# Kernel tuning notes

Hardware: AMD Instinct MI355X
Metric: run time of the kernel (lower is better)

Reference implementation:

```python
import jax, jax.numpy as jnp
import numpy as np

WIN = 30


def setup_inputs() -> dict:
    key = jax.random.key(0)
    ks = jax.random.split(key, 10)
    B, T, N = 16, 3000, 128
    d, hid, K = 64, 128, 32  # d_model, 2*d_model, n_clusters
    s = lambda k, shape, fan: jax.random.normal(k, shape, jnp.float32) / np.float32(np.sqrt(fan))
    return {
        "x_enc": jax.random.normal(ks[0], (B, T, N), jnp.float32),
        "conv1_w": s(ks[1], (32, 1, 5), 5),
        "conv1_b": jnp.zeros((32,), jnp.float32),
        "conv2_w": s(ks[2], (32, 32, 5), 160),
        "conv2_b": jnp.zeros((32,), jnp.float32),
        "proj_w": s(ks[3], (32, d), 32),
        "proj_b": jnp.zeros((d,), jnp.float32),
        "prototypes": s(ks[4], (K, d), d),
        "Wx": s(ks[5], (d, 4 * hid), d),   # stacked gate input weights, order [i,f,o,g]
        "bx": jnp.zeros((4 * hid,), jnp.float32),
        "Wh": s(ks[6], (hid, 4 * hid), hid),  # stacked gate hidden weights
        "bh": jnp.zeros((4 * hid,), jnp.float32),
        "q_t": jax.random.normal(ks[7], (hid,), jnp.float32),
        "q_s": jax.random.normal(ks[8], (d,), jnp.float32),
        "cls_w": s(ks[9], (hid + d, 1), hid + d),
        "cls_b": jnp.zeros((1,), jnp.float32),
    }


def _forward(x_enc, conv1_w, conv1_b, conv2_w, conv2_b, proj_w, proj_b,
             prototypes, Wx, bx, Wh, bh, q_t, q_s, cls_w, cls_b):
    B, T, N = x_enc.shape
    Wn = T // WIN
    xw = x_enc[:, :Wn * WIN].reshape(B, Wn, WIN, N)  # [B,Wn,L,N]

    # --- dynamic FC graphs: per-window correlation ---
    xm = xw - xw.mean(axis=2, keepdims=True)
    cov = jnp.einsum('bwln,bwlm->bwnm', xm, xm) / (WIN - 1 + 1e-8)
    var = jnp.clip(jnp.diagonal(cov, axis1=-2, axis2=-1), 1e-8, None)
    std = jnp.sqrt(var)
    corr = cov / (std[..., :, None] * std[..., None, :])
    corr = jnp.nan_to_num(0.5 * (corr + jnp.swapaxes(corr, -1, -2)), nan=0.0, posinf=0.0, neginf=0.0)
    eyeN = jnp.eye(N, dtype=corr.dtype)
    A_seq = corr * (1.0 - eyeN) + eyeN  # [B,Wn,N,N]

    # --- SignalRep over all windows at once (eval mode: no dropout) ---
    seq = jnp.transpose(xw, (0, 1, 3, 2)).reshape(B * Wn * N, 1, WIN)
    dn = ('NCH', 'OIH', 'NCH')
    h = jax.nn.relu(jax.lax.conv_general_dilated(seq, conv1_w, (1,), [(2, 2)], dimension_numbers=dn) + conv1_b[None, :, None])
    h = jax.nn.relu(jax.lax.conv_general_dilated(h, conv2_w, (1,), [(2, 2)], dimension_numbers=dn) + conv2_b[None, :, None])
    h = h.mean(-1) @ proj_w + proj_b
    Hs = h.reshape(B, Wn, N, -1)  # [B,Wn,N,d]

    # --- attention graph pooling (batched over windows) ---
    S = jax.nn.softmax(jnp.einsum('bwnf,kf->bwnk', Hs, prototypes), axis=-1)
    Xc = jnp.einsum('bwnk,bwnf->bwkf', S, Hs)            # [B,Wn,K,d]
    AS = jnp.einsum('bwnm,bwml->bwnl', A_seq, S)
    Ac = jnp.einsum('bwnk,bwnl->bwkl', S, AS)            # [B,Wn,K,K]
    Ac = 0.5 * (Ac + jnp.swapaxes(Ac, -1, -2))

    # --- normalize pooled adjacency once (shared by all 8 gate GCNs) ---
    K = Ac.shape[-1]
    Ahat = Ac + jnp.eye(K, dtype=Ac.dtype)
    dinv = jnp.clip(Ahat.sum(-1), 1e-8, None) ** -0.5
    An = dinv[..., :, None] * Ahat * dinv[..., None, :]  # D^-1/2 (A+I) D^-1/2

    # --- TGRL: GCLSTM recurrence with p_list=(1,2) skip-averaging ---
    hid = Wh.shape[0]
    Xs = jnp.swapaxes(Xc, 0, 1)  # [Wn,B,K,d]
    As = jnp.swapaxes(An, 0, 1)  # [Wn,B,K,K]
    H0 = jnp.zeros((B, K, hid), Xc.dtype)
    b_all = bx + bh

    def step(carry, inp):
        H, H2, C, t = carry  # H = H_hist[-1], H2 = H_hist[-2]
        X, A = inp
        # H_prev = (H + sum of applicable H_hist[-p]) / (1 + count)
        coef = jnp.where(t == 0, 1.0, 2.0)
        denom = jnp.where(t == 0, 1.0, jnp.where(t == 1, 2.0, 3.0))
        Hp = (coef * H + H2) / denom
        g = jnp.einsum('bkm,bmh->bkh', A, X @ Wx + Hp @ Wh + b_all)  # fused 4 gates
        gi, gf, go, gc = jnp.split(g, 4, axis=-1)
        Cn = jax.nn.sigmoid(gf) * C + jax.nn.sigmoid(gi) * jnp.tanh(gc)
        Hn = jax.nn.sigmoid(go) * jnp.tanh(Cn)
        return (Hn, H, Cn, t + 1), Hn

    _, H_seq = jax.lax.scan(step, (H0, H0, H0, jnp.int32(0)), (Xs, As))
    H_seq = jnp.swapaxes(H_seq, 0, 1)  # [B,Wn,K,hid]

    # --- temporal attention pooling ---
    def attn_pool(Z, q):
        qn = q / (jnp.linalg.norm(q) + 1e-8)
        w = jax.nn.softmax(Z @ qn, axis=1)  # softmax over time
        return jnp.einsum('bw,bwf->bf', w, Z)

    z_graph = attn_pool(H_seq.mean(2), q_t)   # mean over clusters
    z_signal = attn_pool(Hs.mean(2), q_s)     # mean over nodes
    z = jnp.concatenate([z_graph, z_signal], axis=-1)
    return jax.nn.sigmoid(z @ cls_w + cls_b)  # out_dim == 1 (binary)


def reference(x_enc, conv1_w, conv1_b, conv2_w, conv2_b, proj_w, proj_b,
              prototypes, Wx, bx, Wh, bh, q_t, q_s, cls_w, cls_b):
    return _forward(x_enc, conv1_w, conv1_b, conv2_w, conv2_b, proj_w, proj_b,
                    prototypes, Wx, bx, Wh, bh, q_t, q_s, cls_w, cls_b)
```

## Files before the change

kernel.cpp:

```cpp
#include <hip/hip_runtime.h>

#define B_   16
#define T_   3000
#define N_   128
#define WIN_ 30
#define WN_  100
#define D_   64
#define HID_ 128
#define K_   32
#define G4_  512

typedef unsigned short us;
typedef __attribute__((ext_vector_type(8))) short short8;
typedef __attribute__((ext_vector_type(4))) short short4v;
typedef __attribute__((ext_vector_type(4))) float floatx4;

__device__ __forceinline__ us f2bf(float f) {
    unsigned u = __float_as_uint(f);
    u += 0x7fffu + ((u >> 16) & 1u);
    return (us)(u >> 16);
}
__device__ __forceinline__ float bf2f(us h) {
    return __uint_as_float(((unsigned)h) << 16);
}
__device__ __forceinline__ float rcpa(float x) { return __builtin_amdgcn_rcpf(x); }
__device__ __forceinline__ float ex2(float x) { return __builtin_amdgcn_exp2f(x); }
__device__ __forceinline__ void ldsbar() {
    __asm__ volatile("s_waitcnt lgkmcnt(0)\n\ts_barrier" ::: "memory");
}

#define SC_IFO (-1.4426950408889634f)
#define SC_C   (-2.8853900817779268f)

__global__ __launch_bounds__(256) void conv_kernel(
    const float* __restrict__ x, const float* __restrict__ w1,
    const float* __restrict__ b1, const float* __restrict__ w2,
    const float* __restrict__ b2, const float* __restrict__ pw,
    const float* __restrict__ pb, us* __restrict__ Hs)
{
    __shared__ __align__(16) float xs_all[30 * 128];
    __shared__ __align__(16) us h1s[8 * 36 * 40];
    __shared__ __align__(16) float Ms[128 * 40];
    __shared__ __align__(16) us PwT_hi[64 * 40];
    __shared__ __align__(16) us PwT_lo[64 * 40];
    const int tid = threadIdx.x;
    const int win = blockIdx.x;
    const int b = win / WN_, w = win - b * WN_;
    const float* xb = x + ((size_t)b * T_ + (size_t)w * WIN_) * N_;
    const int lane = tid & 63, wv = tid >> 6;
    const int l15 = lane & 15, quad = lane >> 4;

    {
        const float4* xb4 = (const float4*)xb;
        float4* xs4 = (float4*)xs_all;
        for (int i = tid; i < 960; i += 256) xs4[i] = xb4[i];
    }
    for (int i = tid; i < 2048; i += 256) {
        int co = i >> 6, d = i & 63;
        float v = pw[i];
        us hi = f2bf(v);
        PwT_hi[d * 40 + co] = hi;
        PwT_lo[d * 40 + co] = f2bf(v - bf2f(hi));
    }
    for (int i = tid; i < 1920; i += 256) {
        int s = i / 240, r = i % 240;
        int ti = r / 40, c = r % 40;
        int tp = (ti < 2) ? ti : (30 + ti);
        h1s[(s * 36 + tp) * 40 + c] = 0;
    }
    short8 whf[2][5];
    #pragma unroll
    for (int cot = 0; cot < 2; cot++)
        #pragma unroll
        for (int dk = 0; dk < 5; dk++)
            #pragma unroll
            for (int j = 0; j < 8; j++)
                whf[cot][dk][j] = (short)f2bf(w2[(cot * 16 + l15) * 160 + (quad * 8 + j) * 5 + dk]);
    const float b2c0 = b2[l15], b2c1 = b2[16 + l15];
    const int ci2 = lane & 15, th = (lane >> 4) & 1, sloc = lane >> 5;
    float w1ra[5], w1rb[5];
    #pragma unroll
    for (int k = 0; k < 5; k++) {
        w1ra[k] = w1[(2 * ci2) * 5 + k];
        w1rb[k] = w1[(2 * ci2 + 1) * 5 + k];
    }
    const float b1a = b1[2 * ci2], b1b = b1[2 * ci2 + 1];
    float pbv[4];
    #pragma unroll
    for (int nt = 0; nt < 4; nt++) pbv[nt] = pb[nt * 16 + l15];
    ldsbar();

    for (int g = 0; g < 16; g++) {
        const int n1 = g * 8 + wv * 2 + sloc;
        {
            float xr[19];
            #pragma unroll
            for (int u = 0; u < 19; u++) {
                int p = th * 15 - 2 + u;
                xr[u] = ((unsigned)p < 30u) ? xs_all[p * 128 + n1] : 0.f;
            }
            const int rbase = (wv * 2 + sloc) * 36 + 2 + th * 15;
            #pragma unroll
            for (int tt = 0; tt < 15; tt++) {
                float aa = b1a, ab = b1b;
                #pragma unroll
                for (int k = 0; k < 5; k++) {
                    aa += xr[tt + k] * w1ra[k];
                    ab += xr[tt + k] * w1rb[k];
                }
                unsigned pk = (unsigned)f2bf(fmaxf(aa, 0.f))
                            | ((unsigned)f2bf(fmaxf(ab, 0.f)) << 16);
                *(unsigned*)&h1s[(rbase + tt) * 40 + 2 * ci2] = pk;
            }
        }
        __builtin_amdgcn_wave_barrier();
        #pragma unroll
        for (int s2 = 0; s2 < 2; s2++) {
            const int sl = wv * 2 + s2;
            const int nn = g * 8 + sl;
            floatx4 c00 = {b2c0, b2c0, b2c0, b2c0};
            floatx4 c01 = {b2c1, b2c1, b2c1, b2c1};
            floatx4 c10 = {b2c0, b2c0, b2c0, b2c0};
            floatx4 c11 = {b2c1, b2c1, b2c1, b2c1};
            #pragma unroll
            for (int dk = 0; dk < 5; dk++) {
                short8 a0 = *(const short8*)&h1s[(sl * 36 + l15 + dk) * 40 + quad * 8];
                short8 a1 = *(const short8*)&h1s[(sl * 36 + 16 + l15 + dk) * 40 + quad * 8];
                c00 = __builtin_amdgcn_mfma_f32_16x16x32_bf16(a0, whf[0][dk], c00, 0, 0, 0);
                c01 = __builtin_amdgcn_mfma_f32_16x16x32_bf16(a0, whf[1][dk], c01, 0, 0, 0);
                c10 = __builtin_amdgcn_mfma_f32_16x16x32_bf16(a1, whf[0][dk], c10, 0, 0, 0);
                c11 = __builtin_amdgcn_mfma_f32_16x16x32_bf16(a1, whf[1][dk], c11, 0, 0, 0);
            }
            float s0 = 0.f, s1 = 0.f;
            #pragma unroll
            for (int r = 0; r < 4; r++) {
                s0 += fmaxf(c00[r], 0.f);
                s1 += fmaxf(c01[r], 0.f);
                float m0 = (quad * 4 + r < 14) ? fmaxf(c10[r], 0.f) : 0.f;
                float m1 = (quad * 4 + r < 14) ? fmaxf(c11[r], 0.f) : 0.f;
                s0 += m0; s1 += m1;
            }
            s0 += __shfl_xor(s0, 16); s0 += __shfl_xor(s0, 32);
            s1 += __shfl_xor(s1, 16); s1 += __shfl_xor(s1, 32);
            if (quad == 0) {
                Ms[nn * 40 + l15]      = s0 * (1.f / 30.f);
                Ms[nn * 40 + 16 + l15] = s1 * (1.f / 30.f);
            }
        }
        __builtin_amdgcn_wave_barrier();
    }
    ldsbar();
    short8 Ah[2], Al[2];
    #pragma unroll
    for (int i = 0; i < 2; i++) {
        const int mt = wv * 2 + i;
        float4 v0 = *(const float4*)&Ms[(mt * 16 + l15) * 40 + quad * 8];
        float4 v1 = *(const float4*)&Ms[(mt * 16 + l15) * 40 + quad * 8 + 4];
        float vv[8] = {v0.x, v0.y, v0.z, v0.w, v1.x, v1.y, v1.z, v1.w};
        #pragma unroll
        for (int j = 0; j < 8; j++) {
            us hi = f2bf(vv[j]);
            Ah[i][j] = (short)hi;
            Al[i][j] = (short)f2bf(vv[j] - bf2f(hi));
        }
    }
    us* hp = Hs + (size_t)win * 8192;
    #pragma unroll
    for (int id = 0; id < 8; id++) {
        const int i = id >> 2, nt = id & 3;
        short8 Bh = *(const short8*)&PwT_hi[(nt * 16 + l15) * 40 + quad * 8];
        short8 Bl = *(const short8*)&PwT_lo[(nt * 16 + l15) * 40 + quad * 8];
        floatx4 a = {pbv[nt], pbv[nt], pbv[nt], pbv[nt]};
        a = __builtin_amdgcn_mfma_f32_16x16x32_bf16(Ah[i], Bh, a, 0, 0, 0);
        a = __builtin_amdgcn_mfma_f32_16x16x32_bf16(Al[i], Bh, a, 0, 0, 0);
        a = __builtin_amdgcn_mfma_f32_16x16x32_bf16(Ah[i], Bl, a, 0, 0, 0);
        const int mt = wv * 2 + i;
        #pragma unroll
        for (int r = 0; r < 4; r++)
            hp[(mt * 16 + quad * 4 + r) * 64 + nt * 16 + l15] = f2bf(a[r]);
    }
}

__global__ __launch_bounds__(256) void prep_kernel(
    const float* __restrict__ Wh, const float* __restrict__ Wx,
    const float* __restrict__ bx, const float* __restrict__ bh,
    us* __restrict__ WhT, us* __restrict__ WxT, float* __restrict__ bs2)
{
    int i = blockIdx.x * 256 + threadIdx.x;
    if (i < 65536) {
        int jj = i >> 7, h = i & 127;
        float sc = (jj >> 7) == 3 ? SC_C : SC_IFO;
        WhT[i] = f2bf(Wh[h * G4_ + jj] * sc);
    } else if (i < 98304) {
        int j = i - 65536;
        int jj = j >> 6, d = j & 63;
        float sc = (jj >> 7) == 3 ? SC_C : SC_IFO;
        WxT[j] = f2bf(Wx[d * G4_ + jj] * sc);
    } else if (i < 98816) {
        int jj = i - 98304;
        float sc = (jj >> 7) == 3 ? SC_C : SC_IFO;
        bs2[jj] = (bx[jj] + bh[jj]) * sc;
    }
}

__global__ __launch_bounds__(256) void xcwx_kernel(
    const us* __restrict__ Hs, const float* __restrict__ proto,
    const us* __restrict__ WxT, const float* __restrict__ bs2,
    us* __restrict__ S_out, us* __restrict__ XWx, float* __restrict__ Hsm)
{
    __shared__ __align__(16) us Hnd[128 * 72];
    __shared__ __align__(16) us HsT[64 * 136];
    __shared__ __align__(16) us PT_hi[32 * 72];
    __shared__ __align__(16) us SsT_hi[32 * 136];
    __shared__ __align__(16) us XcA_hi[32 * 72];
    __shared__ float bias[512];
    const int tid = threadIdx.x;
    const int win = blockIdx.x;
    const int lane = tid & 63, wv = tid >> 6;
    const int l15 = lane & 15, quad = lane >> 4;

    {
        const uint2* hp = (const uint2*)(Hs + (size_t)win * 8192);
        #pragma unroll
        for (int it = 0; it < 8; it++) {
            int idx4 = tid + 256 * it;
            int n = idx4 >> 4, dpos = (idx4 & 15) * 4;
            uint2 v = hp[idx4];
            *(uint2*)&Hnd[n * 72 + dpos] = v;
            us s0 = (us)(v.x & 0xffff), s1 = (us)(v.x >> 16);
            us s2 = (us)(v.y & 0xffff), s3 = (us)(v.y >> 16);
            HsT[(dpos + 0) * 136 + n] = s0;
            HsT[(dpos + 1) * 136 + n] = s1;
            HsT[(dpos + 2) * 136 + n] = s2;
            HsT[(dpos + 3) * 136 + n] = s3;
        }
        for (int i = tid; i < 2048; i += 256) {
            int k = i >> 6, d = i & 63;
            PT_hi[k * 72 + d] = f2bf(proto[i]);
        }
        for (int i = tid; i < 512; i += 256) bias[i] = bs2[i];
    }
    __syncthreads();
    floatx4 lg[2][2];
    #pragma unroll
    for (int p = 0; p < 2; p++) {
        const int mt = wv * 2 + p;
        #pragma unroll
        for (int kt = 0; kt < 2; kt++) {
            floatx4 a = {0.f, 0.f, 0.f, 0.f};
            #pragma unroll
            for (int kb = 0; kb < 2; kb++) {
                short8 af  = *(const short8*)&Hnd[(mt * 16 + l15) * 72 + kb * 32 + quad * 8];
                short8 bhf = *(const short8*)&PT_hi[(kt * 16 + l15) * 72 + kb * 32 + quad * 8];
                a = __builtin_amdgcn_mfma_f32_16x16x32_bf16(af, bhf, a, 0, 0, 0);
            }
            lg[p][kt] = a;
        }
    }
    #pragma unroll
    for (int p = 0; p < 2; p++) {
        #pragma unroll
        for (int r = 0; r < 4; r++) {
            float v0 = lg[p][0][r], v1 = lg[p][1][r];
            float m = fmaxf(v0, v1);
            #pragma unroll
            for (int off = 8; off; off >>= 1) m = fmaxf(m, __shfl_xor(m, off));
            float e0 = expf(v0 - m), e1 = expf(v1 - m);
            float s = e0 + e1;
            #pragma unroll
            for (int off = 8; off; off >>= 1) s += __shfl_xor(s, off);
            float inv = 1.f / s;
            e0 *= inv; e1 *= inv;
            const int n = (wv * 2 + p) * 16 + quad * 4 + r;
            us h0 = f2bf(e0), h1 = f2bf(e1);
            SsT_hi[l15 * 136 + n]        = h0;
            SsT_hi[(16 + l15) * 136 + n] = h1;
            S_out[(size_t)win * 4096 + n * 32 + l15]      = h0;
            S_out[(size_t)win * 4096 + n * 32 + 16 + l15] = h1;
        }
    }
    __syncthreads();
    {
        const int d = tid >> 2, seg = tid & 3;
        float acc = 0.f;
        const unsigned* hp2 = (const unsigned*)&HsT[d * 136 + seg * 32];
        #pragma unroll
        for (int q = 0; q < 16; q++) {
            unsigned v = hp2[q];
            acc += bf2f((us)(v & 0xffff)) + bf2f((us)(v >> 16));
        }
        acc += __shfl_xor(acc, 1);
        acc += __shfl_xor(acc, 2);
        if (seg == 0) Hsm[(size_t)win * 64 + d] = acc * (1.f / 128.f);
    }
    #pragma unroll
    for (int p = 0; p < 2; p++) {
        const int id = wv * 2 + p, mt = id >> 2, nt = id & 3;
        floatx4 a = {0.f, 0.f, 0.f, 0.f};
        #pragma unroll
        for (int kb = 0; kb < 4; kb++) {
            short8 ah = *(const short8*)&SsT_hi[(mt * 16 + l15) * 136 + kb * 32 + quad * 8];
            short8 bf_ = *(const short8*)&HsT[(nt * 16 + l15) * 136 + kb * 32 + quad * 8];
            a = __builtin_amdgcn_mfma_f32_16x16x32_bf16(ah, bf_, a, 0, 0, 0);
        }
        #pragma unroll
        for (int r = 0; r < 4; r++) {
            const int k = mt * 16 + quad * 4 + r, d = nt * 16 + l15;
            XcA_hi[k * 72 + d] = f2bf(a[r]);
        }
    }
    __syncthreads();
    short8 Ah[2][2];
    #pragma unroll
    for (int mt = 0; mt < 2; mt++)
        #pragma unroll
        for (int kb = 0; kb < 2; kb++)
            Ah[mt][kb] = *(const short8*)&XcA_hi[(mt * 16 + l15) * 72 + kb * 32 + quad * 8];
    #pragma unroll 1
    for (int i = 0; i < 8; i++) {
        const int nt = wv + 4 * i;
        const float bv = bias[nt * 16 + l15];
        floatx4 acc[2];
        acc[0] = (floatx4){bv, bv, bv, bv};
        acc[1] = (floatx4){bv, bv, bv, bv};
        #pragma unroll
        for (int kb = 0; kb < 2; kb++) {
            short8 wh8 = *(const short8*)&WxT[(size_t)(nt * 16 + l15) * 64 + kb * 32 + quad * 8];
            #pragma unroll
            for (int mt = 0; mt < 2; mt++)
                acc[mt] = __builtin_amdgcn_mfma_f32_16x16x32_bf16(Ah[mt][kb], wh8, acc[mt], 0, 0, 0);
        }
        #pragma unroll
        for (int mt = 0; mt < 2; mt++) {
            uint2 pk;
            pk.x = (unsigned)f2bf(acc[mt][0]) | ((unsigned)f2bf(acc[mt][1]) << 16);
            pk.y = (unsigned)f2bf(acc[mt][2]) | ((unsigned)f2bf(acc[mt][3]) << 16);
            ((uint2*)XWx)[((size_t)win * 64 + mt * 32 + nt) * 64 + lane] = pk;
        }
    }
}

__global__ __launch_bounds__(256) void corr_kernel(
    const float* __restrict__ x, const us* __restrict__ S_bf,
    us* __restrict__ An, us* __restrict__ XWx)
{
    __shared__ __align__(16) float xs[30 * 128];
    __shared__ __align__(16) us SsT[32 * 136];
    __shared__ __align__(16) us pool[21760];
    __shared__ float Acs[32 * 33];
    __shared__ __align__(16) us AnL[32 * 40];
    __shared__ float sinv[128];
    __shared__ float dinv[32];
    us* XA  = (us*)xs;
    us* CB  = pool;
    us* AST = pool + 17408;
    us* XWT = pool;
    const int tid = threadIdx.x;
    const int win = blockIdx.x;
    const int b = win / WN_, w = win - b * WN_;
    const float* xb = x + ((size_t)b * T_ + (size_t)w * WIN_) * N_;
    const int lane = tid & 63, wv = tid >> 6;
    const int l15 = lane & 15, quad = lane >> 4;
    const float inv29 = 1.f / (WIN_ - 1 + 1e-8f);

    {
        const float4* xb4 = (const float4*)xb;
        float4* xs4 = (float4*)xs;
        for (int i = tid; i < 960; i += 256) xs4[i] = xb4[i];
    }
    {
        const uint2* sp = (const uint2*)(S_bf + (size_t)win * 4096);
        for (int i4 = tid; i4 < 1024; i4 += 256) {
            uint2 v = sp[i4];
            int n = i4 >> 3, k0 = (i4 & 7) * 4;
            SsT[(k0 + 0) * 136 + n] = (us)(v.x & 0xffff);
            SsT[(k0 + 1) * 136 + n] = (us)(v.x >> 16);
            SsT[(k0 + 2) * 136 + n] = (us)(v.y & 0xffff);
            SsT[(k0 + 3) * 136 + n] = (us)(v.y >> 16);
        }
    }
    __syncthreads();
    float xr[30];
    if (tid < 128) {
        const int n = tid;
        float mean = 0.f;
        #pragma unroll
        for (int l = 0; l < 30; l++) { xr[l] = xs[l * 128 + n]; mean += xr[l]; }
        mean *= (1.f / 30.f);
        float var = 0.f;
        #pragma unroll
        for (int l = 0; l < 30; l++) {
            float v = xr[l] - mean;
            var += v * v;
            xr[l] = v;
        }
        var *= inv29;
        sinv[tid] = rsqrtf(fmaxf(var, 1e-8f));
    }
    __syncthreads();
    if (tid < 128) {
        #pragma unroll
        for (int l = 0; l < 30; l++) XA[tid * 40 + l] = f2bf(xr[l]);
        XA[tid * 40 + 30] = 0; XA[tid * 40 + 31] = 0;
    }
    __syncthreads();
    #pragma unroll 1
    for (int q = 0; q < 16; q++) {
        const int id = wv * 16 + q, mt = id >> 3, nt = id & 7;
        short8 a = *(const short8*)&XA[(mt * 16 + l15) * 40 + quad * 8];
        short8 bb = *(const short8*)&XA[(nt * 16 + l15) * 40 + quad * 8];
        floatx4 d = {0.f, 0.f, 0.f, 0.f};
        d = __builtin_amdgcn_mfma_f32_16x16x32_bf16(a, bb, d, 0, 0, 0);
        const int m = nt * 16 + l15;
        const float sm = sinv[m];
        #pragma unroll
        for (int r = 0; r < 4; r++) {
            const int n = mt * 16 + quad * 4 + r;
            float v = d[r] * inv29 * sinv[n] * sm;
            if (n == m) v = 1.f;
            CB[n * 136 + m] = f2bf(v);
        }
    }
    __syncthreads();
    #pragma unroll 1
    for (int q = 0; q < 4; q++) {
        const int id = wv * 4 + q, mt = id >> 1, lt = id & 1;
        floatx4 d = {0.f, 0.f, 0.f, 0.f};
        #pragma unroll
        for (int kb = 0; kb < 4; kb++) {
            short8 a = *(const short8*)&CB[(mt * 16 + l15) * 136 + kb * 32 + quad * 8];
            short8 bb = *(const short8*)&SsT[(lt * 16 + l15) * 136 + kb * 32 + quad * 8];
            d = __builtin_amdgcn_mfma_f32_16x16x32_bf16(a, bb, d, 0, 0, 0);
        }
        const int l = lt * 16 + l15;
        #pragma unroll
        for (int r = 0; r < 4; r++)
            AST[l * 136 + mt * 16 + quad * 4 + r] = f2bf(d[r]);
    }
    __syncthreads();
    {
        const int kt = wv >> 1, lt = wv & 1;
        floatx4 d = {0.f, 0.f, 0.f, 0.f};
        #pragma unroll
        for (int kb = 0; kb < 4; kb++) {
            short8 a = *(const short8*)&SsT[(kt * 16 + l15) * 136 + kb * 32 + quad * 8];
            short8 bb = *(const short8*)&AST[(lt * 16 + l15) * 136 + kb * 32 + quad * 8];
            d = __builtin_amdgcn_mfma_f32_16x16x32_bf16(a, bb, d, 0, 0, 0);
        }
        #pragma unroll
        for (int r = 0; r < 4; r++)
            Acs[(kt * 16 + quad * 4 + r) * 33 + lt * 16 + l15] = d[r];
    }
    __syncthreads();
    float symv[4];
    {
        int l = tid & 31, kb = tid >> 5;
        for (int r = 0; r < 4; r++) {
            int k = kb + 8 * r;
            symv[r] = 0.5f * (Acs[k * 33 + l] + Acs[l * 33 + k]) + ((k == l) ? 1.f : 0.f);
        }
    }
    __syncthreads();
    {
        int l = tid & 31, kb = tid >> 5;
        for (int r = 0; r < 4; r++) Acs[(kb + 8 * r) * 33 + l] = symv[r];
    }
    __syncthreads();
    if (tid < K_) {
        float s = 0.f;
        for (int l = 0; l < K_; l++) s += Acs[tid * 33 + l];
        dinv[tid] = rsqrtf(fmaxf(s, 1e-8f));
    }
    __syncthreads();
    us* Anw = An + (size_t)win * K_ * K_;
    for (int i = tid; i < K_ * K_; i += 256) {
        int k = i >> 5, l = i & 31;
        us v = f2bf(dinv[k] * Acs[k * 33 + l] * dinv[l]);
        Anw[i] = v;
        AnL[k * 40 + l] = v;
    }
    __syncthreads();
    {
        const uint4* xw4 = (const uint4*)((const uint2*)XWx + (size_t)win * 4096);
        for (int i2 = tid; i2 < 2048; i2 += 256) {
            uint4 v = xw4[i2];
            int i = i2 * 2;
            int tile = i >> 6, lane2 = i & 63;
            int mt2 = tile >> 5, nt2 = tile & 31;
            int jj = nt2 * 16 + (lane2 & 15);
            int m0 = mt2 * 16 + (lane2 >> 4) * 4;
            *(uint2*)&XWT[jj * 40 + m0] = make_uint2(v.x, v.y);
            int jj1 = nt2 * 16 + ((lane2 + 1) & 15);
            int m01 = mt2 * 16 + (((lane2 + 1) >> 4)) * 4;
            *(uint2*)&XWT[jj1 * 40 + m01] = make_uint2(v.z, v.w);
        }
    }
    __syncthreads();
    short8 anA[2];
    anA[0] = *(const short8*)&AnL[l15 * 40 + quad * 8];
    anA[1] = *(const short8*)&AnL[(16 + l15) * 40 + quad * 8];
    #pragma unroll 1
    for (int i = 0; i < 8; i++) {
        const int nt = wv + 4 * i;
        short8 bfr = *(const short8*)&XWT[(nt * 16 + l15) * 40 + quad * 8];
        #pragma unroll
        for (int mt2 = 0; mt2 < 2; mt2++) {
            floatx4 a = {0.f, 0.f, 0.f, 0.f};
            a = __builtin_amdgcn_mfma_f32_16x16x32_bf16(anA[mt2], bfr, a, 0, 0, 0);
            uint2 pk;
            pk.x = (unsigned)f2bf(a[0]) | ((unsigned)f2bf(a[1]) << 16);
            pk.y = (unsigned)f2bf(a[2]) | ((unsigned)f2bf(a[3]) << 16);
            ((uint2*)XWx)[((size_t)win * 64 + mt2 * 32 + nt) * 64 + lane] = pk;
        }
    }
}

__global__ __launch_bounds__(1024) void scan_kernel(
    const us* __restrict__ An_bf,
    const us* __restrict__ AXWx,
    const us* __restrict__ WhT,
    float* __restrict__ Hsq2)
{
    __shared__ __align__(16) us HpT[2][128 * 40];
    __shared__ __align__(16) us P_lds[32 * 136];

    const int tid  = threadIdx.x;
    const int lane = tid & 63;
    const int wv   = tid >> 6;
    const int b    = blockIdx.x;
    const int l15  = lane & 15, quad = lane >> 4;
    const int mt   = wv >> 3, hb = wv & 7;

    short8 Bw[4][4];
    #pragma unroll
    for (int g4 = 0; g4 < 4; g4++) {
        const int jj = g4 * 128 + hb * 16 + l15;
        #pragma unroll
        for (int kb = 0; kb < 4; kb++)
            Bw[g4][kb] = *(const short8*)&WhT[(size_t)jj * 128 + kb * 32 + quad * 8];
    }
    float Cst[4] = {0.f, 0.f, 0.f, 0.f};
    float Hst[4] = {0.f, 0.f, 0.f, 0.f};
    float H2t[4] = {0.f, 0.f, 0.f, 0.f};

    for (int i = tid; i < 2560; i += 1024) ((unsigned*)HpT[0])[i] = 0;

    const size_t bt0 = (size_t)b * WN_;
    const uint2* xq = (const uint2*)AXWx + (bt0 * 64 + (size_t)mt * 32 + hb) * 64 + lane;
    const us*   anp = An_bf + bt0 * 1024 + (size_t)(mt * 16 + l15) * 32 + quad * 8;

    uint2 xw[4];
    #pragma unroll
    for (int g4 = 0; g4 < 4; g4++) xw[g4] = xq[g4 * 512];
    short8 anf = *(const short8*)anp;

    #pragma unroll 1
    for (int t = 0; t < WN_; t++) {
        const int buf = t & 1;
        ldsbar();
        short8 hpB = *(const short8*)&HpT[buf][(hb * 16 + l15) * 40 + quad * 8];
        floatx4 Pa = {0.f, 0.f, 0.f, 0.f};
        Pa = __builtin_amdgcn_mfma_f32_16x16x32_bf16(anf, hpB, Pa, 0, 0, 0);
        #pragma unroll
        for (int r = 0; r < 4; r++)
            P_lds[(mt * 16 + quad * 4 + r) * 136 + hb * 16 + l15] = f2bf(Pa[r]);
        floatx4 gacc[4];
        #pragma unroll
        for (int g4 = 0; g4 < 4; g4++) {
            gacc[g4][0] = __uint_as_float(xw[g4].x << 16);
            gacc[g4][1] = __uint_as_float(xw[g4].x & 0xffff0000u);
            gacc[g4][2] = __uint_as_float(xw[g4].y << 16);
            gacc[g4][3] = __uint_as_float(xw[g4].y & 0xffff0000u);
        }
        if (t + 1 < WN_) { xq += 4096; anp += 1024; }
        #pragma unroll
        for (int g4 = 0; g4 < 4; g4++) xw[g4] = xq[g4 * 512];
        anf = *(const short8*)anp;
        ldsbar();
        #pragma unroll
        for (int kb = 0; kb < 4; kb++) {
            short8 pA = *(const short8*)&P_lds[(mt * 16 + l15) * 136 + kb * 32 + quad * 8];
            #pragma unroll
            for (int g4 = 0; g4 < 4; g4++)
                gacc[g4] = __builtin_amdgcn_mfma_f32_16x16x32_bf16(pA, Bw[g4][kb], gacc[g4], 0, 0, 0);
        }
        #pragma unroll
        for (int r = 0; r < 4; r++) {
            float si = rcpa(1.f + ex2(gacc[0][r]));
            float sf = rcpa(1.f + ex2(gacc[1][r]));
            float so = rcpa(1.f + ex2(gacc[2][r]));
            float tc = 2.f * rcpa(1.f + ex2(gacc[3][r])) - 1.f;
            float cn = sf * Cst[r] + si * tc;
            float tn = 2.f * rcpa(1.f + ex2(cn * SC_C)) - 1.f;
            float hn = so * tn;
            Cst[r] = cn;
            H2t[r] = Hst[r];
            Hst[r] = hn;
        }
        if (t + 1 < WN_) {
            const float dninv = (t + 1 == 1) ? 0.5f : (1.f / 3.f);
            short4v hv;
            #pragma unroll
            for (int r = 0; r < 4; r++)
                hv[r] = (short)f2bf((2.f * Hst[r] + H2t[r]) * dninv);
            *(short4v*)&HpT[buf ^ 1][(hb * 16 + l15) * 40 + mt * 16 + quad * 4] = hv;
        }
        {
            float s = Hst[0] + Hst[1] + Hst[2] + Hst[3];
            s += __shfl_xor(s, 16); s += __shfl_xor(s, 32);
            if (quad == 0)
                Hsq2[((bt0 + t) * 2 + mt) * HID_ + hb * 16 + l15] = s;
        }
    }
}

__global__ __launch_bounds__(128) void final_kernel(
    const float* __restrict__ Hsq2, const float* __restrict__ Hsm,
    const float* __restrict__ q_t, const float* __restrict__ q_s,
    const float* __restrict__ cls_w, const float* __restrict__ cls_b,
    float* __restrict__ out)
{
    __shared__ float red[128];
    __shared__ float wt[WN_];
    const int b = blockIdx.x, tid = threadIdx.x;
    float v = q_t[tid];
    red[tid] = v * v;
    __syncthreads();
    for (int off = 64; off; off >>= 1) {
        if (tid < off) red[tid] += red[tid + off];
        __syncthreads();
    }
    const float qtn = sqrtf(red[0]) + 1e-8f;
    __syncthreads();
    float v2 = (tid < D_) ? q_s[tid] : 0.f;
    red[tid] = v2 * v2;
    __syncthreads();
    for (int off = 64; off; off >>= 1) {
        if (tid < off) red[tid] += red[tid + off];
        __syncthreads();
    }
    const float qsn = sqrtf(red[0]) + 1e-8f;
    __syncthreads();
    float sc_t = -1e30f;
    if (tid < WN_) {
        float s = 0.f;
        const float* zr = Hsq2 + ((size_t)b * WN_ + tid) * (2 * HID_);
        for (int h = 0; h < HID_; h++) s += (zr[h] + zr[HID_ + h]) * q_t[h];
        sc_t = s * (1.f / 32.f) / qtn;
    }
    red[tid] = sc_t;
    __syncthreads();
    for (int off = 64; off; off >>= 1) {
        if (tid < off) red[tid] = fmaxf(red[tid], red[tid + off]);
        __syncthreads();
    }
    const float mt_ = red[0];
    __syncthreads();
    float e_t = (tid < WN_) ? expf(sc_t - mt_) : 0.f;
    red[tid] = e_t;
    __syncthreads();
    for (int off = 64; off; off >>= 1) {
        if (tid < off) red[tid] += red[tid + off];
        __syncthreads();
    }
    const float sinv_t = 1.f / red[0];
    __syncthreads();
    if (tid < WN_) wt[tid] = e_t * sinv_t;
    __syncthreads();
    float part = 0.f;
    {
        float z = 0.f;
        for (int w = 0; w < WN_; w++) {
            const float* p = Hsq2 + ((size_t)b * WN_ + w) * (2 * HID_);
            z += wt[w] * (p[tid] + p[HID_ + tid]);
        }
        part += z * (1.f / 32.f) * cls_w[tid];
    }
    __syncthreads();
    float sc_s = -1e30f;
    if (tid < WN_) {
        float s = 0.f;
        const float* zr = Hsm + ((size_t)b * WN_ + tid) * D_;
        for (int dd = 0; dd < D_; dd++) s += zr[dd] * q_s[dd];
        sc_s = s / qsn;
    }
    red[tid] = sc_s;
    __syncthreads();
    for (int off = 64; off; off >>= 1) {
        if (tid < off) red[tid] = fmaxf(red[tid], red[tid + off]);
        __syncthreads();
    }
    const float ms_ = red[0];
    __syncthreads();
    float e_s = (tid < WN_) ? expf(sc_s - ms_) : 0.f;
    red[tid] = e_s;
    __syncthreads();
    for (int off = 64; off; off >>= 1) {
        if (tid < off) red[tid] += red[tid + off];
        __syncthreads();
    }
    const float sinv_s = 1.f / red[0];
    __syncthreads();
    if (tid < WN_) wt[tid] = e_s * sinv_s;
    __syncthreads();
    if (tid < D_) {
        float z = 0.f;
        for (int w = 0; w < WN_; w++)
            z += wt[w] * Hsm[((size_t)b * WN_ + w) * D_ + tid];
        part += z * cls_w[HID_ + tid];
    }
    red[tid] = part;
    __syncthreads();
    for (int off = 64; off; off >>= 1) {
        if (tid < off) red[tid] += red[tid + off];
        __syncthreads();
    }
    if (tid == 0) out[b] = 1.f / (1.f + expf(-(red[0] + cls_b[0])));
}

extern "C" void kernel_launch(void* const* d_in, const int* in_sizes, int n_in,
                              void* d_out, int out_size, void* d_ws, size_t ws_size,
                              hipStream_t stream)
{
    (void)in_sizes; (void)n_in; (void)out_size; (void)ws_size;
    const float* x     = (const float*)d_in[0];
    const float* w1    = (const float*)d_in[1];
    const float* b1    = (const float*)d_in[2];
    const float* w2    = (const float*)d_in[3];
    const float* b2    = (const float*)d_in[4];
    const float* pw    = (const float*)d_in[5];
    const float* pb    = (const float*)d_in[6];
    const float* proto = (const float*)d_in[7];
    const float* Wx    = (const float*)d_in[8];
    const float* bx    = (const float*)d_in[9];
    const float* Wh    = (const float*)d_in[10];
    const float* bh    = (const float*)d_in[11];
    const float* q_t   = (const float*)d_in[12];
    const float* q_s   = (const float*)d_in[13];
    const float* clw   = (const float*)d_in[14];
    const float* clb   = (const float*)d_in[15];

    float* ws = (float*)d_ws;
    us*    Hs_bf  = (us*)d_ws;
    us*    S_bf   = (us*)(ws + 6553600);
    us*    XWx    = (us*)(ws + 9830400);
    us*    An_bf  = (us*)(ws + 22937600);
    float* Hsm    = ws + 23756800;
    float* Hsq2   = ws + 6553600;
    us*    WhT    = (us*)(ws + 24064000);
    us*    WxT    = (us*)(ws + 24096768);
    float* bs2    = ws + 24129536;

    prep_kernel<<<386, 256, 0, stream>>>(Wh, Wx, bx, bh, WhT, WxT, bs2);
    conv_kernel<<<B_ * WN_, 256, 0, stream>>>(x, w1, b1, w2, b2, pw, pb, Hs_bf);
    xcwx_kernel<<<B_ * WN_, 256, 0, stream>>>(Hs_bf, proto, WxT, bs2,
                                              S_bf, XWx, Hsm);
    corr_kernel<<<B_ * WN_, 256, 0, stream>>>(x, S_bf, An_bf, XWx);
    scan_kernel<<<B_, 1024, 0, stream>>>(An_bf, XWx, WhT, Hsq2);
    final_kernel<<<B_, 128, 0, stream>>>(Hsq2, Hsm, q_t, q_s, clw, clb,
                                         (float*)d_out);
}
```

Before: 547.7 us.

## Fuse conv and cluster-assignment/Wx projection kernels via shared LDS pool

Merges the conv kernel and the xcwx kernel into one per-window kernel. The projected signal features now stay in LDS (written directly into Hnd and HsT) and are never written to and reread from global memory. This removes one launch and the Hs round trip, and reuses LDS through an aliased pool. In exchange the fused kernel uses more LDS (about 69KB), which may lower occupancy.

```diff
diff --git a/kernel.cpp b/kernel.cpp
--- a/kernel.cpp
+++ b/kernel.cpp
@@ -32,17 +32,27 @@
 #define SC_IFO (-1.4426950408889634f)
 #define SC_C   (-2.8853900817779268f)
 
-__global__ __launch_bounds__(256) void conv_kernel(
+__global__ __launch_bounds__(256) void convx_kernel(
     const float* __restrict__ x, const float* __restrict__ w1,
     const float* __restrict__ b1, const float* __restrict__ w2,
     const float* __restrict__ b2, const float* __restrict__ pw,
-    const float* __restrict__ pb, us* __restrict__ Hs)
+    const float* __restrict__ pb, const float* __restrict__ proto,
+    const us* __restrict__ WxT, const float* __restrict__ bs2,
+    us* __restrict__ S_out, us* __restrict__ XWx, float* __restrict__ Hsm)
 {
-    __shared__ __align__(16) float xs_all[30 * 128];
-    __shared__ __align__(16) us h1s[8 * 36 * 40];
-    __shared__ __align__(16) float Ms[128 * 40];
-    __shared__ __align__(16) us PwT_hi[64 * 40];
-    __shared__ __align__(16) us PwT_lo[64 * 40];
+    __shared__ __align__(16) us pool[34560];
+    float* xs_all = (float*)pool;
+    us*    h1s    = pool + 7680;
+    float* Ms     = (float*)(pool + 19200);
+    us*    PwT_hi = pool + 29440;
+    us*    PwT_lo = pool + 32000;
+    us*    Hnd    = pool;
+    us*    HsT    = pool + 9216;
+    us*    PT_hi  = pool + 17920;
+    us*    SsT_hi = pool + 20224;
+    us*    XcA_hi = pool + 24576;
+    float* bias   = (float*)(pool + 26880);
+
     const int tid = threadIdx.x;
     const int win = blockIdx.x;
     const int b = win / WN_, w = win - b * WN_;
@@ -150,34 +160,147 @@
         __builtin_amdgcn_wave_barrier();
     }
     ldsbar();
-    short8 Ah[2], Al[2];
+    {
+        short8 Ah[2], Al[2];
+        #pragma unroll
+        for (int i = 0; i < 2; i++) {
+            const int mt = wv * 2 + i;
+            float4 v0 = *(const float4*)&Ms[(mt * 16 + l15) * 40 + quad * 8];
+            float4 v1 = *(const float4*)&Ms[(mt * 16 + l15) * 40 + quad * 8 + 4];
+            float vv[8] = {v0.x, v0.y, v0.z, v0.w, v1.x, v1.y, v1.z, v1.w};
+            #pragma unroll
+            for (int j = 0; j < 8; j++) {
+                us hi = f2bf(vv[j]);
+                Ah[i][j] = (short)hi;
+                Al[i][j] = (short)f2bf(vv[j] - bf2f(hi));
+            }
+        }
+        #pragma unroll
+        for (int id = 0; id < 8; id++) {
+            const int i = id >> 2, nt = id & 3;
+            short8 Bh = *(const short8*)&PwT_hi[(nt * 16 + l15) * 40 + quad * 8];
+            short8 Bl = *(const short8*)&PwT_lo[(nt * 16 + l15) * 40 + quad * 8];
+            floatx4 a = {pbv[nt], pbv[nt], pbv[nt], pbv[nt]};
+            a = __builtin_amdgcn_mfma_f32_16x16x32_bf16(Ah[i], Bh, a, 0, 0, 0);
+            a = __builtin_amdgcn_mfma_f32_16x16x32_bf16(Al[i], Bh, a, 0, 0, 0);
+            a = __builtin_amdgcn_mfma_f32_16x16x32_bf16(Ah[i], Bl, a, 0, 0, 0);
+            const int mt = wv * 2 + i;
+            const int d_ = nt * 16 + l15;
+            #pragma unroll
+            for (int r = 0; r < 4; r++) {
+                const int n_ = mt * 16 + quad * 4 + r;
+                us hv = f2bf(a[r]);
+                Hnd[n_ * 72 + d_] = hv;
+                HsT[d_ * 136 + n_] = hv;
+            }
+        }
+    }
+    ldsbar();
+    for (int i = tid; i < 2048; i += 256) {
+        int k = i >> 6, d = i & 63;
+        PT_hi[k * 72 + d] = f2bf(proto[i]);
+    }
+    for (int i = tid; i < 512; i += 256) bias[i] = bs2[i];
+    __syncthreads();
+
+    floatx4 lg[2][2];
     #pragma unroll
-    for (int i = 0; i < 2; i++) {
-        const int mt = wv * 2 + i;
-        float4 v0 = *(const float4*)&Ms[(mt * 16 + l15) * 40 + quad * 8];
-        float4 v1 = *(const float4*)&Ms[(mt * 16 + l15) * 40 + quad * 8 + 4];
-        float vv[8] = {v0.x, v0.y, v0.z, v0.w, v1.x, v1.y, v1.z, v1.w};
-        #pragma unroll
-        for (int j = 0; j < 8; j++) {
-            us hi = f2bf(vv[j]);
-            Ah[i][j] = (short)hi;
-            Al[i][j] = (short)f2bf(vv[j] - bf2f(hi));
-        }
-    }
-    us* hp = Hs + (size_t)win * 8192;
+    for (int p = 0; p < 2; p++) {
+        const int mt = wv * 2 + p;
+        #pragma unroll
+        for (int kt = 0; kt < 2; kt++) {
+            floatx4 a = {0.f, 0.f, 0.f, 0.f};
+            #pragma unroll
+            for (int kb = 0; kb < 2; kb++) {
+                short8 af  = *(const short8*)&Hnd[(mt * 16 + l15) * 72 + kb * 32 + quad * 8];
+                short8 bhf = *(const short8*)&PT_hi[(kt * 16 + l15) * 72 + kb * 32 + quad * 8];
+                a = __builtin_amdgcn_mfma_f32_16x16x32_bf16(af, bhf, a, 0, 0, 0);
+            }
+            lg[p][kt] = a;
+        }
+    }
     #pragma unroll
-    for (int id = 0; id < 8; id++) {
-        const int i = id >> 2, nt = id & 3;
-        short8 Bh = *(const short8*)&PwT_hi[(nt * 16 + l15) * 40 + quad * 8];
-        short8 Bl = *(const short8*)&PwT_lo[(nt * 16 + l15) * 40 + quad * 8];
-        floatx4 a = {pbv[nt], pbv[nt], pbv[nt], pbv[nt]};
-        a = __builtin_amdgcn_mfma_f32_16x16x32_bf16(Ah[i], Bh, a, 0, 0, 0);
-        a = __builtin_amdgcn_mfma_f32_16x16x32_bf16(Al[i], Bh, a, 0, 0, 0);
-        a = __builtin_amdgcn_mfma_f32_16x16x32_bf16(Ah[i], Bl, a, 0, 0, 0);
-        const int mt = wv * 2 + i;
-        #pragma unroll
-        for (int r = 0; r < 4; r++)
-            hp[(mt * 16 + quad * 4 + r) * 64 + nt * 16 + l15] = f2bf(a[r]);
+    for (int p = 0; p < 2; p++) {
+        #pragma unroll
+        for (int r = 0; r < 4; r++) {
+            float v0 = lg[p][0][r], v1 = lg[p][1][r];
+            float m = fmaxf(v0, v1);
+            #pragma unroll
+            for (int off = 8; off; off >>= 1) m = fmaxf(m, __shfl_xor(m, off));
+            float e0 = expf(v0 - m), e1 = expf(v1 - m);
+            float s = e0 + e1;
+            #pragma unroll
+            for (int off = 8; off; off >>= 1) s += __shfl_xor(s, off);
+            float inv = 1.f / s;
+            e0 *= inv; e1 *= inv;
+            const int n = (wv * 2 + p) * 16 + quad * 4 + r;
+            us h0 = f2bf(e0), h1 = f2bf(e1);
+            SsT_hi[l15 * 136 + n]        = h0;
+            SsT_hi[(16 + l15) * 136 + n] = h1;
+            S_out[(size_t)win * 4096 + n * 32 + l15]      = h0;
+            S_out[(size_t)win * 4096 + n * 32 + 16 + l15] = h1;
+        }
+    }
+    __syncthreads();
+    {
+        const int d = tid >> 2, seg = tid & 3;
+        float acc = 0.f;
+        const unsigned* hp2 = (const unsigned*)&HsT[d * 136 + seg * 32];
+        #pragma unroll
+        for (int q = 0; q < 16; q++) {
+            unsigned v = hp2[q];
+            acc += bf2f((us)(v & 0xffff)) + bf2f((us)(v >> 16));
+        }
+        acc += __shfl_xor(acc, 1);
+        acc += __shfl_xor(acc, 2);
+        if (seg == 0) Hsm[(size_t)win * 64 + d] = acc * (1.f / 128.f);
+    }
+    #pragma unroll
+    for (int p = 0; p < 2; p++) {
+        const int id = wv * 2 + p, mt = id >> 2, nt = id & 3;
+        floatx4 a = {0.f, 0.f, 0.f, 0.f};
+        #pragma unroll
+        for (int kb = 0; kb < 4; kb++) {
+            short8 ah = *(const short8*)&SsT_hi[(mt * 16 + l15) * 136 + kb * 32 + quad * 8];
+            short8 bf_ = *(const short8*)&HsT[(nt * 16 + l15) * 136 + kb * 32 + quad * 8];
+            a = __builtin_amdgcn_mfma_f32_16x16x32_bf16(ah, bf_, a, 0, 0, 0);
+        }
+        #pragma unroll
+        for (int r = 0; r < 4; r++) {
+            const int k = mt * 16 + quad * 4 + r, d = nt * 16 + l15;
+            XcA_hi[k * 72 + d] = f2bf(a[r]);
+        }
+    }
+    __syncthreads();
+    {
+        short8 Axc[2][2];
+        #pragma unroll
+        for (int mt = 0; mt < 2; mt++)
+            #pragma unroll
+            for (int kb = 0; kb < 2; kb++)
+                Axc[mt][kb] = *(const short8*)&XcA_hi[(mt * 16 + l15) * 72 + kb * 32 + quad * 8];
+        #pragma unroll 1
+        for (int i = 0; i < 8; i++) {
+            const int nt = wv + 4 * i;
+            const float bv = bias[nt * 16 + l15];
+            floatx4 acc[2];
+            acc[0] = (floatx4){bv, bv, bv, bv};
+            acc[1] = (floatx4){bv, bv, bv, bv};
+            #pragma unroll
+            for (int kb = 0; kb < 2; kb++) {
+                short8 wh8 = *(const short8*)&WxT[(size_t)(nt * 16 + l15) * 64 + kb * 32 + quad * 8];
+                #pragma unroll
+                for (int mt = 0; mt < 2; mt++)
+                    acc[mt] = __builtin_amdgcn_mfma_f32_16x16x32_bf16(Axc[mt][kb], wh8, acc[mt], 0, 0, 0);
+            }
+            #pragma unroll
+            for (int mt = 0; mt < 2; mt++) {
+                uint2 pk;
+                pk.x = (unsigned)f2bf(acc[mt][0]) | ((unsigned)f2bf(acc[mt][1]) << 16);
+                pk.y = (unsigned)f2bf(acc[mt][2]) | ((unsigned)f2bf(acc[mt][3]) << 16);
+                ((uint2*)XWx)[((size_t)win * 64 + mt * 32 + nt) * 64 + lane] = pk;
+            }
+        }
     }
 }
 
@@ -200,143 +323,6 @@
         int jj = i - 98304;
         float sc = (jj >> 7) == 3 ? SC_C : SC_IFO;
         bs2[jj] = (bx[jj] + bh[jj]) * sc;
-    }
-}
-
-__global__ __launch_bounds__(256) void xcwx_kernel(
-    const us* __restrict__ Hs, const float* __restrict__ proto,
-    const us* __restrict__ WxT, const float* __restrict__ bs2,
-    us* __restrict__ S_out, us* __restrict__ XWx, float* __restrict__ Hsm)
-{
-    __shared__ __align__(16) us Hnd[128 * 72];
-    __shared__ __align__(16) us HsT[64 * 136];
-    __shared__ __align__(16) us PT_hi[32 * 72];
-    __shared__ __align__(16) us SsT_hi[32 * 136];
-    __shared__ __align__(16) us XcA_hi[32 * 72];
-    __shared__ float bias[512];
-    const int tid = threadIdx.x;
-    const int win = blockIdx.x;
-    const int lane = tid & 63, wv = tid >> 6;
-    const int l15 = lane & 15, quad = lane >> 4;
-
-    {
-        const uint2* hp = (const uint2*)(Hs + (size_t)win * 8192);
-        #pragma unroll
-        for (int it = 0; it < 8; it++) {
-            int idx4 = tid + 256 * it;
-            int n = idx4 >> 4, dpos = (idx4 & 15) * 4;
-            uint2 v = hp[idx4];
-            *(uint2*)&Hnd[n * 72 + dpos] = v;
-            us s0 = (us)(v.x & 0xffff), s1 = (us)(v.x >> 16);
-            us s2 = (us)(v.y & 0xffff), s3 = (us)(v.y >> 16);
-            HsT[(dpos + 0) * 136 + n] = s0;
-            HsT[(dpos + 1) * 136 + n] = s1;
-            HsT[(dpos + 2) * 136 + n] = s2;
-            HsT[(dpos + 3) * 136 + n] = s3;
-        }
-        for (int i = tid; i < 2048; i += 256) {
-            int k = i >> 6, d = i & 63;
-            PT_hi[k * 72 + d] = f2bf(proto[i]);
-        }
-        for (int i = tid; i < 512; i += 256) bias[i] = bs2[i];
-    }
-    __syncthreads();
-    floatx4 lg[2][2];
-    #pragma unroll
-    for (int p = 0; p < 2; p++) {
-        const int mt = wv * 2 + p;
-        #pragma unroll
-        for (int kt = 0; kt < 2; kt++) {
-            floatx4 a = {0.f, 0.f, 0.f, 0.f};
-            #pragma unroll
-            for (int kb = 0; kb < 2; kb++) {
-                short8 af  = *(const short8*)&Hnd[(mt * 16 + l15) * 72 + kb * 32 + quad * 8];
-                short8 bhf = *(const short8*)&PT_hi[(kt * 16 + l15) * 72 + kb * 32 + quad * 8];
-                a = __builtin_amdgcn_mfma_f32_16x16x32_bf16(af, bhf, a, 0, 0, 0);
-            }
-            lg[p][kt] = a;
-        }
-    }
-    #pragma unroll
-    for (int p = 0; p < 2; p++) {
-        #pragma unroll
-        for (int r = 0; r < 4; r++) {
-            float v0 = lg[p][0][r], v1 = lg[p][1][r];
-            float m = fmaxf(v0, v1);
-            #pragma unroll
-            for (int off = 8; off; off >>= 1) m = fmaxf(m, __shfl_xor(m, off));
-            float e0 = expf(v0 - m), e1 = expf(v1 - m);
-            float s = e0 + e1;
-            #pragma unroll
-            for (int off = 8; off; off >>= 1) s += __shfl_xor(s, off);
-            float inv = 1.f / s;
-            e0 *= inv; e1 *= inv;
-            const int n = (wv * 2 + p) * 16 + quad * 4 + r;
-            us h0 = f2bf(e0), h1 = f2bf(e1);
-            SsT_hi[l15 * 136 + n]        = h0;
-            SsT_hi[(16 + l15) * 136 + n] = h1;
-            S_out[(size_t)win * 4096 + n * 32 + l15]      = h0;
-            S_out[(size_t)win * 4096 + n * 32 + 16 + l15] = h1;
-        }
-    }
-    __syncthreads();
-    {
-        const int d = tid >> 2, seg = tid & 3;
-        float acc = 0.f;
-        const unsigned* hp2 = (const unsigned*)&HsT[d * 136 + seg * 32];
-        #pragma unroll
-        for (int q = 0; q < 16; q++) {
-            unsigned v = hp2[q];
-            acc += bf2f((us)(v & 0xffff)) + bf2f((us)(v >> 16));
-        }
-        acc += __shfl_xor(acc, 1);
-        acc += __shfl_xor(acc, 2);
-        if (seg == 0) Hsm[(size_t)win * 64 + d] = acc * (1.f / 128.f);
-    }
-    #pragma unroll
-    for (int p = 0; p < 2; p++) {
-        const int id = wv * 2 + p, mt = id >> 2, nt = id & 3;
-        floatx4 a = {0.f, 0.f, 0.f, 0.f};
-        #pragma unroll
-        for (int kb = 0; kb < 4; kb++) {
-            short8 ah = *(const short8*)&SsT_hi[(mt * 16 + l15) * 136 + kb * 32 + quad * 8];
-            short8 bf_ = *(const short8*)&HsT[(nt * 16 + l15) * 136 + kb * 32 + quad * 8];
-            a = __builtin_amdgcn_mfma_f32_16x16x32_bf16(ah, bf_, a, 0, 0, 0);
-        }
-        #pragma unroll
-        for (int r = 0; r < 4; r++) {
-            const int k = mt * 16 + quad * 4 + r, d = nt * 16 + l15;
-            XcA_hi[k * 72 + d] = f2bf(a[r]);
-        }
-    }
-    __syncthreads();
-    short8 Ah[2][2];
-    #pragma unroll
-    for (int mt = 0; mt < 2; mt++)
-        #pragma unroll
-        for (int kb = 0; kb < 2; kb++)
-            Ah[mt][kb] = *(const short8*)&XcA_hi[(mt * 16 + l15) * 72 + kb * 32 + quad * 8];
-    #pragma unroll 1
-    for (int i = 0; i < 8; i++) {
-        const int nt = wv + 4 * i;
-        const float bv = bias[nt * 16 + l15];
-        floatx4 acc[2];
-        acc[0] = (floatx4){bv, bv, bv, bv};
-        acc[1] = (floatx4){bv, bv, bv, bv};
-        #pragma unroll
-        for (int kb = 0; kb < 2; kb++) {
-            short8 wh8 = *(const short8*)&WxT[(size_t)(nt * 16 + l15) * 64 + kb * 32 + quad * 8];
-            #pragma unroll
-            for (int mt = 0; mt < 2; mt++)
-                acc[mt] = __builtin_amdgcn_mfma_f32_16x16x32_bf16(Ah[mt][kb], wh8, acc[mt], 0, 0, 0);
-        }
-        #pragma unroll
-        for (int mt = 0; mt < 2; mt++) {
-            uint2 pk;
-            pk.x = (unsigned)f2bf(acc[mt][0]) | ((unsigned)f2bf(acc[mt][1]) << 16);
-            pk.y = (unsigned)f2bf(acc[mt][2]) | ((unsigned)f2bf(acc[mt][3]) << 16);
-            ((uint2*)XWx)[((size_t)win * 64 + mt * 32 + nt) * 64 + lane] = pk;
-        }
     }
 }
 
@@ -741,7 +727,6 @@
     const float* clb   = (const float*)d_in[15];
 
     float* ws = (float*)d_ws;
-    us*    Hs_bf  = (us*)d_ws;
     us*    S_bf   = (us*)(ws + 6553600);
     us*    XWx    = (us*)(ws + 9830400);
     us*    An_bf  = (us*)(ws + 22937600);
@@ -752,9 +737,9 @@
     float* bs2    = ws + 24129536;
 
     prep_kernel<<<386, 256, 0, stream>>>(Wh, Wx, bx, bh, WhT, WxT, bs2);
-    conv_kernel<<<B_ * WN_, 256, 0, stream>>>(x, w1, b1, w2, b2, pw, pb, Hs_bf);
-    xcwx_kernel<<<B_ * WN_, 256, 0, stream>>>(Hs_bf, proto, WxT, bs2,
-                                              S_bf, XWx, Hsm);
+    convx_kernel<<<B_ * WN_, 256, 0, stream>>>(x, w1, b1, w2, b2, pw, pb,
+                                               proto, WxT, bs2,
+                                               S_bf, XWx, Hsm);
     corr_kernel<<<B_ * WN_, 256, 0, stream>>>(x, S_bf, An_bf, XWx);
     scan_kernel<<<B_, 1024, 0, stream>>>(An_bf, XWx, WhT, Hsq2);
     final_kernel<<<B_, 128, 0, stream>>>(Hsq2, Hsm, q_t, q_s, clw, clb,
```

New measurement: 540.0 us. About the same (-1.4%).
